# Optimization experiments

Hardware: AMD Instinct MI355X
Metric: run time of the kernel (lower is better)

## Reference

```python
import jax, jax.numpy as jnp
import numpy as np

N = 20000      # nodes
E = 320000     # edges (avg in-degree 16)
R = 100        # relation types
F = 256        # in_ent_feats == out_ent_feats == in_rel_feats
H = 8          # heads
D = F // H     # head dim = 32
HOP = 5        # PPR hops
ALPHA = 0.1
SLOPE = 0.2    # LeakyReLU negative slope


def _ln(x, g, b, eps=1e-5):
    m = x.mean(-1, keepdims=True)
    v = ((x - m) ** 2).mean(-1, keepdims=True)
    return (x - m) / jnp.sqrt(v + eps) * g + b


def setup_inputs() -> dict:
    key = jax.random.key(0)
    ks = jax.random.split(key, 12)
    s = 1.0 / np.sqrt(F)
    ent_feat = jax.random.normal(ks[0], (N, F), jnp.float32)
    rel_feat = jax.random.normal(ks[1], (R, F), jnp.float32)
    W_head = jax.random.normal(ks[2], (F, F), jnp.float32) * s
    W_tail = jax.random.normal(ks[3], (F, F), jnp.float32) * s
    W_ent = jax.random.normal(ks[4], (F, F), jnp.float32) * s
    W_rel = jax.random.normal(ks[5], (F, F), jnp.float32) * s
    attn = jax.random.normal(ks[6], (1, H, D), jnp.float32) * s
    ln_ent_g = jnp.ones((F,), jnp.float32); ln_ent_b = jnp.zeros((F,), jnp.float32)
    ln_rel_g = jnp.ones((F,), jnp.float32); ln_rel_b = jnp.zeros((F,), jnp.float32)
    ln_ff_g = jnp.ones((F,), jnp.float32); ln_ff_b = jnp.zeros((F,), jnp.float32)
    W1 = jax.random.normal(ks[7], (F, 4 * F), jnp.float32) * s
    b1 = jnp.zeros((4 * F,), jnp.float32)
    W2 = jax.random.normal(ks[8], (4 * F, F), jnp.float32) * (0.5 * s)
    b2 = jnp.zeros((F,), jnp.float32)
    src = jax.random.randint(ks[9], (E,), 0, N, dtype=jnp.int32)
    # every node must have in-degree >= 1 (DGL raises on 0-in-degree nodes)
    dst = jnp.concatenate([jnp.arange(N, dtype=jnp.int32),
                           jax.random.randint(ks[10], (E - N,), 0, N, dtype=jnp.int32)])
    rid = jax.random.randint(ks[11], (E,), 0, R, dtype=jnp.int32)
    return {"ent_feat": ent_feat, "rel_feat": rel_feat,
            "W_head": W_head, "W_tail": W_tail, "W_ent": W_ent, "W_rel": W_rel,
            "attn": attn,
            "ln_ent_g": ln_ent_g, "ln_ent_b": ln_ent_b,
            "ln_rel_g": ln_rel_g, "ln_rel_b": ln_rel_b,
            "ln_ff_g": ln_ff_g, "ln_ff_b": ln_ff_b,
            "W1": W1, "b1": b1, "W2": W2, "b2": b2,
            "src": src, "dst": dst, "rid": rid}


def reference(ent_feat, rel_feat, W_head, W_tail, W_ent, W_rel, attn,
              ln_ent_g, ln_ent_b, ln_rel_g, ln_rel_b, ln_ff_g, ln_ff_b,
              W1, b1, W2, b2, src, dst, rid):
    n = ent_feat.shape[0]
    x = _ln(ent_feat, ln_ent_g, ln_ent_b)                 # [N,F]
    fh = (x @ W_head).reshape(n, H, D)                    # 'eh'
    ftl = (x @ W_tail).reshape(n, H, D)                   # 'et'
    fen = (x @ W_ent).reshape(n, H, D)                    # 'ft'
    r = _ln(rel_feat, ln_rel_g, ln_rel_b)
    fr = (r @ W_rel).reshape(-1, H, D)[rid]               # [E,H,D]
    # relational edge attention score
    e = jax.nn.leaky_relu(fh[src] * ftl[dst] * fr, SLOPE)
    e = (e * attn).sum(-1)                                # [E,H]
    # e_mul_v with log in-degree, scaled by head_dim
    deg = jax.ops.segment_sum(jnp.ones((src.shape[0],), e.dtype), dst, num_segments=n)
    e = e * (jnp.log(deg)[dst])[:, None] / D
    # edge softmax over incoming edges of each dst node, per head
    m = jax.lax.stop_gradient(jax.ops.segment_max(e, dst, num_segments=n))
    ex = jnp.exp(e - m[dst])
    denom = jax.ops.segment_sum(ex, dst, num_segments=n)
    a = ex / denom[dst]                                   # [E,H]
    # PPR-style diffusion aggregation
    feat0 = fen
    feat = fen
    for _ in range(HOP):
        msg = feat[src] * a[:, :, None]                   # [E,H,D]
        agg = jax.ops.segment_sum(msg, dst, num_segments=n)
        feat = (1.0 - ALPHA) * agg + ALPHA * feat0
    # residual (Identity since in_ent_feats == out_ent_feats)
    rst = feat + ent_feat.reshape(n, H, D)
    rst = rst.reshape(n, F)
    # position-wise feed-forward with pre-LN and residual
    y = _ln(rst, ln_ff_g, ln_ff_b)
    ff = jax.nn.relu(y @ W1 + b1) @ W2 + b2
    return ff + rst
```

## Files before the change

kernel.cpp:

```cpp
#include <hip/hip_runtime.h>

#define N_NODES 20000
#define N_EDGES 320000
#define N_REL   100
#define FDIM    256
#define NHEAD   8
#define HDIM    32
#define SCAN_BLOCKS ((N_NODES + 255) / 256)

using short8 = __attribute__((ext_vector_type(8))) short;
using f32x4  = __attribute__((ext_vector_type(4))) float;

__device__ inline unsigned short f2bf(float f) {
    union { float f; unsigned int u; } v; v.f = f;
    unsigned int r = v.u + 0x7fff + ((v.u >> 16) & 1);
    return (unsigned short)(r >> 16);
}
__device__ inline float bf2f(unsigned short u) {
    union { unsigned int i; float f; } v; v.i = ((unsigned int)u) << 16; return v.f;
}
__device__ inline float4 bf4(ushort4 u) {
    return make_float4(bf2f(u.x), bf2f(u.y), bf2f(u.z), bf2f(u.w));
}
__device__ inline void unpack8(float* d, uint4 u) {
    union { unsigned int u; float f; } t;
    t.u = u.x << 16;         d[0] = t.f;
    t.u = u.x & 0xffff0000u; d[1] = t.f;
    t.u = u.y << 16;         d[2] = t.f;
    t.u = u.y & 0xffff0000u; d[3] = t.f;
    t.u = u.z << 16;         d[4] = t.f;
    t.u = u.z & 0xffff0000u; d[5] = t.f;
    t.u = u.w << 16;         d[6] = t.f;
    t.u = u.w & 0xffff0000u; d[7] = t.f;
}
__device__ inline void fma8(float* acc, uint4 u, float w) {
    union { unsigned int u; float f; } t;
    t.u = u.x << 16;         acc[0] += w * t.f;
    t.u = u.x & 0xffff0000u; acc[1] += w * t.f;
    t.u = u.y << 16;         acc[2] += w * t.f;
    t.u = u.y & 0xffff0000u; acc[3] += w * t.f;
    t.u = u.z << 16;         acc[4] += w * t.f;
    t.u = u.z & 0xffff0000u; acc[5] += w * t.f;
    t.u = u.w << 16;         acc[6] += w * t.f;
    t.u = u.w & 0xffff0000u; acc[7] += w * t.f;
}
__device__ __forceinline__ void g2lds16(const unsigned short* g, unsigned short* l) {
    __builtin_amdgcn_global_load_lds(
        (const __attribute__((address_space(1))) unsigned int*)g,
        (__attribute__((address_space(3))) unsigned int*)l,
        16, 0, 0);
}

__global__ __launch_bounds__(64) void ln_bf16_kernel(
    const float* __restrict__ in, const float* __restrict__ g,
    const float* __restrict__ b, unsigned short* __restrict__ out, int rows)
{
    int row = blockIdx.x;
    if (row >= rows) return;
    int tid = threadIdx.x;
    const float4 v = *(const float4*)(in + (size_t)row * FDIM + tid * 4);
    float s = v.x + v.y + v.z + v.w;
    float q = v.x * v.x + v.y * v.y + v.z * v.z + v.w * v.w;
    #pragma unroll
    for (int d = 1; d < 64; d <<= 1) { s += __shfl_xor(s, d); q += __shfl_xor(q, d); }
    float mean = s * (1.0f / FDIM);
    float var  = q * (1.0f / FDIM) - mean * mean;
    float inv  = rsqrtf(var + 1e-5f);
    float4 gg = *(const float4*)(g + tid * 4);
    float4 bb = *(const float4*)(b + tid * 4);
    ushort4 o;
    o.x = f2bf((v.x - mean) * inv * gg.x + bb.x);
    o.y = f2bf((v.y - mean) * inv * gg.y + bb.y);
    o.z = f2bf((v.z - mean) * inv * gg.z + bb.z);
    o.w = f2bf((v.w - mean) * inv * gg.w + bb.w);
    *(ushort4*)(out + (size_t)row * FDIM + tid * 4) = o;
}

__global__ __launch_bounds__(64) void rst_ln_kernel(
    const unsigned short* __restrict__ feat, const float* __restrict__ ent,
    const float* __restrict__ g, const float* __restrict__ b,
    float* __restrict__ rst, unsigned short* __restrict__ y)
{
    int row = blockIdx.x;
    int tid = threadIdx.x;
    const float4 f = bf4(*(const ushort4*)(feat + (size_t)row * FDIM + tid * 4));
    const float4 e = *(const float4*)(ent + (size_t)row * FDIM + tid * 4);
    float4 r;
    r.x = f.x + e.x; r.y = f.y + e.y; r.z = f.z + e.z; r.w = f.w + e.w;
    *(float4*)(rst + (size_t)row * FDIM + tid * 4) = r;
    float s = r.x + r.y + r.z + r.w;
    float q = r.x * r.x + r.y * r.y + r.z * r.z + r.w * r.w;
    #pragma unroll
    for (int d = 1; d < 64; d <<= 1) { s += __shfl_xor(s, d); q += __shfl_xor(q, d); }
    float mean = s * (1.0f / FDIM);
    float var  = q * (1.0f / FDIM) - mean * mean;
    float inv  = rsqrtf(var + 1e-5f);
    float4 gg = *(const float4*)(g + tid * 4);
    float4 bb = *(const float4*)(b + tid * 4);
    ushort4 o;
    o.x = f2bf((r.x - mean) * inv * gg.x + bb.x);
    o.y = f2bf((r.y - mean) * inv * gg.y + bb.y);
    o.z = f2bf((r.z - mean) * inv * gg.z + bb.z);
    o.w = f2bf((r.w - mean) * inv * gg.w + bb.w);
    *(ushort4*)(y + (size_t)row * FDIM + tid * 4) = o;
}

__global__ void transpose_bf16_kernel(const float* __restrict__ W,
                                      unsigned short* __restrict__ Wt, int K, int N)
{
    int idx = blockIdx.x * 256 + threadIdx.x;
    if (idx >= K * N) return;
    int n = idx / K, k = idx - n * K;
    Wt[idx] = f2bf(W[(size_t)k * N + n]);
}

__global__ __launch_bounds__(256) void mfma_gemm_bt(
    const unsigned short* __restrict__ A, const unsigned short* __restrict__ Bt,
    const float* __restrict__ bias, const float* __restrict__ add,
    float* __restrict__ Cf, unsigned short* __restrict__ Cb,
    int M, int K, int N, int relu)
{
    __shared__ unsigned short As[128 * 32];
    __shared__ unsigned short Bs[128 * 32];
    int tid  = threadIdx.x;
    int wave = tid >> 6, lane = tid & 63;
    int quad = lane >> 4, l16 = lane & 15;
    int m0 = blockIdx.x * 128, n0 = blockIdx.y * 128;
    int wr = (wave >> 1) * 64, wc = (wave & 1) * 64;

    f32x4 acc[4][4] = {};

    int cA = tid, cB = tid + 256;
    int rA0 = cA >> 2, kA0 = (cA & 3) * 8;
    int rB0 = cB >> 2, kB0 = (cB & 3) * 8;
    int rA = m0 + rA0; if (rA >= M) rA = M - 1;
    int rB = m0 + rB0; if (rB >= M) rB = M - 1;
    const unsigned short* gA0 = A + (size_t)rA * K + kA0;
    const unsigned short* gA1 = A + (size_t)rB * K + kB0;
    const unsigned short* gB0 = Bt + (size_t)(n0 + rA0) * K + kA0;
    const unsigned short* gB1 = Bt + (size_t)(n0 + rB0) * K + kB0;

    for (int k0 = 0; k0 < K; k0 += 32) {
        g2lds16(gA0 + k0, As + cA * 8);
        g2lds16(gA1 + k0, As + cB * 8);
        g2lds16(gB0 + k0, Bs + cA * 8);
        g2lds16(gB1 + k0, Bs + cB * 8);
        __syncthreads();
        short8 af[4], bfr[4];
        #pragma unroll
        for (int i = 0; i < 4; ++i)
            af[i] = *(const short8*)(As + (wr + i * 16 + l16) * 32 + quad * 8);
        #pragma unroll
        for (int j = 0; j < 4; ++j)
            bfr[j] = *(const short8*)(Bs + (wc + j * 16 + l16) * 32 + quad * 8);
        #pragma unroll
        for (int i = 0; i < 4; ++i)
            #pragma unroll
            for (int j = 0; j < 4; ++j)
                acc[i][j] = __builtin_amdgcn_mfma_f32_16x16x32_bf16(
                    af[i], bfr[j], acc[i][j], 0, 0, 0);
        __syncthreads();
    }

    #pragma unroll
    for (int i = 0; i < 4; ++i) {
        #pragma unroll
        for (int j = 0; j < 4; ++j) {
            int col = n0 + wc + j * 16 + l16;
            float bsv = bias ? bias[col] : 0.0f;
            #pragma unroll
            for (int r = 0; r < 4; ++r) {
                int row = m0 + wr + i * 16 + quad * 4 + r;
                if (row < M) {
                    float v = acc[i][j][r] + bsv;
                    if (relu) v = fmaxf(v, 0.0f);
                    if (add)  v += add[(size_t)row * N + col];
                    if (Cf) Cf[(size_t)row * N + col] = v;
                    else    Cb[(size_t)row * N + col] = f2bf(v);
                }
            }
        }
    }
}

__global__ __launch_bounds__(256) void mfma_gemm64_bt(
    const unsigned short* __restrict__ A, const unsigned short* __restrict__ Bt,
    const float* __restrict__ bias, const float* __restrict__ add,
    float* __restrict__ Cf, int M, int K, int N)
{
    __shared__ unsigned short As[64 * 32];
    __shared__ unsigned short Bs[128 * 32];
    int tid  = threadIdx.x;
    int wave = tid >> 6, lane = tid & 63;
    int quad = lane >> 4, l16 = lane & 15;
    int m0 = blockIdx.x * 64, n0 = blockIdx.y * 128;
    int wc = wave * 32;

    f32x4 acc[4][2] = {};

    int rA0 = tid >> 2, kA0 = (tid & 3) * 8;
    int cB0 = tid, cB1 = tid + 256;
    int rB0 = cB0 >> 2, kB0 = (cB0 & 3) * 8;
    int rB1 = cB1 >> 2, kB1 = (cB1 & 3) * 8;
    int rA = m0 + rA0; if (rA >= M) rA = M - 1;
    const unsigned short* gA  = A + (size_t)rA * K + kA0;
    const unsigned short* gB0 = Bt + (size_t)(n0 + rB0) * K + kB0;
    const unsigned short* gB1 = Bt + (size_t)(n0 + rB1) * K + kB1;

    for (int k0 = 0; k0 < K; k0 += 32) {
        g2lds16(gA + k0,  As + tid * 8);
        g2lds16(gB0 + k0, Bs + cB0 * 8);
        g2lds16(gB1 + k0, Bs + cB1 * 8);
        __syncthreads();
        short8 af[4], bfr[2];
        #pragma unroll
        for (int i = 0; i < 4; ++i)
            af[i] = *(const short8*)(As + (i * 16 + l16) * 32 + quad * 8);
        #pragma unroll
        for (int j = 0; j < 2; ++j)
            bfr[j] = *(const short8*)(Bs + (wc + j * 16 + l16) * 32 + quad * 8);
        #pragma unroll
        for (int i = 0; i < 4; ++i)
            #pragma unroll
            for (int j = 0; j < 2; ++j)
                acc[i][j] = __builtin_amdgcn_mfma_f32_16x16x32_bf16(
                    af[i], bfr[j], acc[i][j], 0, 0, 0);
        __syncthreads();
    }

    #pragma unroll
    for (int i = 0; i < 4; ++i) {
        #pragma unroll
        for (int j = 0; j < 2; ++j) {
            int col = n0 + wc + j * 16 + l16;
            float bsv = bias ? bias[col] : 0.0f;
            #pragma unroll
            for (int r = 0; r < 4; ++r) {
                int row = m0 + i * 16 + quad * 4 + r;
                if (row < M) {
                    float v = acc[i][j][r] + bsv;
                    if (add) v += add[(size_t)row * N + col];
                    Cf[(size_t)row * N + col] = v;
                }
            }
        }
    }
}

__global__ void count_kernel(const int* __restrict__ dst, int* __restrict__ deg, int E)
{
    int i = blockIdx.x * blockDim.x + threadIdx.x;
    if (i < E) atomicAdd(&deg[dst[i]], 1);
}

__global__ __launch_bounds__(256) void scan1_kernel(
    const int* __restrict__ deg, int* __restrict__ offsets, int* __restrict__ bsum, int n)
{
    __shared__ int tmp[256];
    int tid = threadIdx.x;
    int i = blockIdx.x * 256 + tid;
    int v = (i < n) ? deg[i] : 0;
    tmp[tid] = v;
    __syncthreads();
    for (int d = 1; d < 256; d <<= 1) {
        int u = (tid >= d) ? tmp[tid - d] : 0;
        __syncthreads();
        tmp[tid] += u;
        __syncthreads();
    }
    if (i < n) offsets[i] = tmp[tid] - v;
    if (tid == 255) bsum[blockIdx.x] = tmp[255];
}

__global__ __launch_bounds__(128) void scan2_kernel(int* __restrict__ bsum, int nb)
{
    __shared__ int tmp[128];
    int tid = threadIdx.x;
    int v = (tid < nb) ? bsum[tid] : 0;
    tmp[tid] = v;
    __syncthreads();
    for (int d = 1; d < 128; d <<= 1) {
        int u = (tid >= d) ? tmp[tid - d] : 0;
        __syncthreads();
        tmp[tid] += u;
        __syncthreads();
    }
    if (tid < nb) bsum[tid] = tmp[tid] - v;
}

__global__ __launch_bounds__(256) void scan3_kernel(
    const int* __restrict__ deg, int* __restrict__ offsets,
    const int* __restrict__ bsum, int* __restrict__ cursor,
    float* __restrict__ logdeg, int n, int E)
{
    int i = blockIdx.x * 256 + threadIdx.x;
    if (i < n) {
        int o = offsets[i] + bsum[blockIdx.x];
        offsets[i] = o;
        cursor[i]  = o;
        logdeg[i]  = logf((float)deg[i]);
    }
    if (i == 0) offsets[n] = E;
}

__global__ void scatter_kernel(const int* __restrict__ dst, const int* __restrict__ src,
                               const int* __restrict__ rid, int* __restrict__ cursor,
                               int* __restrict__ csr_src, int* __restrict__ csr_rid, int E)
{
    int i = blockIdx.x * blockDim.x + threadIdx.x;
    if (i < E) {
        int p = atomicAdd(&cursor[dst[i]], 1);
        csr_src[p] = src[i];
        csr_rid[p] = rid[i];
    }
}

__global__ __launch_bounds__(256) void edge_score_csr_kernel(
    const unsigned short* __restrict__ proj,
    const unsigned short* __restrict__ frel,
    const float* __restrict__ attn,
    const int* __restrict__ csr_src, const int* __restrict__ csr_rid,
    const int* __restrict__ offsets, const float* __restrict__ logdeg,
    float* __restrict__ csr_a, int n)
{
    int node = blockIdx.x * 4 + (threadIdx.x >> 6);
    if (node >= n) return;
    int tid = threadIdx.x & 63;
    int g = tid >> 4, li = tid & 15;
    int start = offsets[node], end = offsets[node + 1];
    float scale = logdeg[node] * (1.0f / 32.0f);

    float tv[16], at[16];
    {
        const unsigned short* tp = proj + (size_t)node * 768 + 256 + li * 16;
        uint4 a0 = *(const uint4*)tp, a1 = *(const uint4*)(tp + 8);
        unpack8(tv, a0); unpack8(tv + 8, a1);
        const float4* ap = (const float4*)(attn + li * 16);
        float4 f;
        f = ap[0]; at[0] = f.x; at[1] = f.y; at[2]  = f.z; at[3]  = f.w;
        f = ap[1]; at[4] = f.x; at[5] = f.y; at[6]  = f.z; at[7]  = f.w;
        f = ap[2]; at[8] = f.x; at[9] = f.y; at[10] = f.z; at[11] = f.w;
        f = ap[3]; at[12] = f.x; at[13] = f.y; at[14] = f.z; at[15] = f.w;
    }

    float denom = 0.f;
    for (int p = start; p < end; p += 8) {
        int  pe[2]; bool va[2]; uint4 h0[2], h1[2], r0[2], r1[2];
        #pragma unroll
        for (int t = 0; t < 2; ++t) {
            pe[t] = p + t * 4 + g;
            va[t] = pe[t] < end;
            int q = va[t] ? pe[t] : end - 1;
            int s = csr_src[q], r = csr_rid[q];
            const unsigned short* hp = proj + (size_t)s * 768 + li * 16;
            const unsigned short* rp = frel + (size_t)r * FDIM + li * 16;
            h0[t] = *(const uint4*)hp; h1[t] = *(const uint4*)(hp + 8);
            r0[t] = *(const uint4*)rp; r1[t] = *(const uint4*)(rp + 8);
        }
        #pragma unroll
        for (int t = 0; t < 2; ++t) {
            float hv[16], rv[16];
            unpack8(hv, h0[t]); unpack8(hv + 8, h1[t]);
            unpack8(rv, r0[t]); unpack8(rv + 8, r1[t]);
            float sum = 0.f;
            #pragma unroll
            for (int k = 0; k < 16; ++k) {
                float m = hv[k] * tv[k] * rv[k];
                m = (m > 0.f) ? m : 0.2f * m;
                sum += m * at[k];
            }
            sum += __shfl_xor(sum, 1);
            float ex = expf(sum * scale);
            if (va[t] && ((li & 1) == 0)) {
                csr_a[(size_t)pe[t] * NHEAD + (li >> 1)] = ex;
                denom += ex;
            }
        }
    }
    denom += __shfl_xor(denom, 16);
    denom += __shfl_xor(denom, 32);
    float dh = __shfl(denom, 2 * (tid & 7));
    for (int i = start * NHEAD + tid; i < end * NHEAD; i += 64)
        csr_a[i] = csr_a[i] / dh;
}

__global__ __launch_bounds__(256) void diffuse_kernel(
    const unsigned short* __restrict__ fin, int fin_stride,
    const unsigned short* __restrict__ feat0,
    const float* __restrict__ a, const int* __restrict__ csr_src,
    const int* __restrict__ offsets, unsigned short* __restrict__ fout, int n)
{
    int node = blockIdx.x * 4 + (threadIdx.x >> 6);
    if (node >= n) return;
    int tid = threadIdx.x & 63;
    int g = tid >> 4, li = tid & 15;
    int hh = li >> 1;
    int start = offsets[node], end = offsets[node + 1];
    float acc[16] = {};

    for (int p = start; p < end; p += 16) {
        uint4 u0[4], u1[4]; float w[4];
        #pragma unroll
        for (int t = 0; t < 4; ++t) {
            int pe = p + t * 4 + g;
            int q = (pe < end) ? pe : end - 1;
            int s = csr_src[q];
            w[t] = (pe < end) ? a[(size_t)q * NHEAD + hh] : 0.0f;
            const unsigned short* rp = fin + (size_t)s * fin_stride + li * 16;
            u0[t] = *(const uint4*)(rp);
            u1[t] = *(const uint4*)(rp + 8);
        }
        #pragma unroll
        for (int t = 0; t < 4; ++t) {
            fma8(acc + 0, u0[t], w[t]);
            fma8(acc + 8, u1[t], w[t]);
        }
    }
    #pragma unroll
    for (int k = 0; k < 16; ++k) {
        acc[k] += __shfl_xor(acc[k], 16);
        acc[k] += __shfl_xor(acc[k], 32);
    }
    if (g == 0) {
        const unsigned short* f0p = feat0 + (size_t)node * 768 + li * 16;
        uint4 f0a = *(const uint4*)(f0p);
        uint4 f0b = *(const uint4*)(f0p + 8);
        float f0[16];
        unpack8(f0, f0a); unpack8(f0 + 8, f0b);
        unsigned short o[16];
        #pragma unroll
        for (int k = 0; k < 16; ++k) o[k] = f2bf(0.9f * acc[k] + 0.1f * f0[k]);
        uint4* dst4 = (uint4*)(fout + (size_t)node * FDIM + li * 16);
        dst4[0] = *(uint4*)(o);
        dst4[1] = *(uint4*)(o + 8);
    }
}

extern "C" void kernel_launch(void* const* d_in, const int* in_sizes, int n_in,
                              void* d_out, int out_size, void* d_ws, size_t ws_size,
                              hipStream_t stream)
{
    const float* ent_feat = (const float*)d_in[0];
    const float* rel_feat = (const float*)d_in[1];
    const float* W_head   = (const float*)d_in[2];
    const float* W_tail   = (const float*)d_in[3];
    const float* W_ent    = (const float*)d_in[4];
    const float* W_rel    = (const float*)d_in[5];
    const float* attn     = (const float*)d_in[6];
    const float* ln_ent_g = (const float*)d_in[7];
    const float* ln_ent_b = (const float*)d_in[8];
    const float* ln_rel_g = (const float*)d_in[9];
    const float* ln_rel_b = (const float*)d_in[10];
    const float* ln_ff_g  = (const float*)d_in[11];
    const float* ln_ff_b  = (const float*)d_in[12];
    const float* W1       = (const float*)d_in[13];
    const float* b1       = (const float*)d_in[14];
    const float* W2       = (const float*)d_in[15];
    const float* b2       = (const float*)d_in[16];
    const int*   src      = (const int*)d_in[17];
    const int*   dst      = (const int*)d_in[18];
    const int*   rid      = (const int*)d_in[19];
    float* out = (float*)d_out;

    char* base = (char*)d_ws;
    auto carve = [&](size_t bytes) { char* p = base; base += (bytes + 255) & ~(size_t)255; return p; };
    unsigned short* xb    = (unsigned short*)carve((size_t)N_NODES * FDIM * 2);
    unsigned short* projb = (unsigned short*)carve((size_t)N_NODES * 768 * 2);
    unsigned short* rlnb  = (unsigned short*)carve((size_t)N_REL * FDIM * 2);
    unsigned short* frelb = (unsigned short*)carve((size_t)N_REL * FDIM * 2);
    unsigned short* WtP   = (unsigned short*)carve((size_t)768 * FDIM * 2);
    unsigned short* WtR   = (unsigned short*)carve((size_t)FDIM * FDIM * 2);
    unsigned short* W1t   = (unsigned short*)carve((size_t)1024 * FDIM * 2);
    unsigned short* W2t   = (unsigned short*)carve((size_t)FDIM * 1024 * 2);
    unsigned short* hb0   = (unsigned short*)carve((size_t)N_NODES * FDIM * 2);
    unsigned short* hb1   = (unsigned short*)carve((size_t)N_NODES * FDIM * 2);
    unsigned short* yb    = (unsigned short*)carve((size_t)N_NODES * FDIM * 2);
    unsigned short* t1b   = (unsigned short*)carve((size_t)N_NODES * 1024 * 2);
    float* rst     = (float*)carve((size_t)N_NODES * FDIM * 4);
    float* csr_a   = (float*)carve(((size_t)N_EDGES * NHEAD + 256) * 4);
    int*   csr_src = (int*)carve((size_t)(N_EDGES + 64) * 4);
    int*   csr_rid = (int*)carve((size_t)(N_EDGES + 64) * 4);
    int*   deg     = (int*)carve((size_t)N_NODES * 4);
    float* logdeg  = (float*)carve((size_t)N_NODES * 4);
    int*   offsets = (int*)carve((size_t)(N_NODES + 1) * 4);
    int*   cursor  = (int*)carve((size_t)N_NODES * 4);
    int*   bsum    = (int*)carve((size_t)SCAN_BLOCKS * 4);

    hipMemsetAsync(deg, 0, (size_t)N_NODES * 4, stream);

    ln_bf16_kernel<<<N_NODES, 64, 0, stream>>>(ent_feat, ln_ent_g, ln_ent_b, xb, N_NODES);
    ln_bf16_kernel<<<N_REL, 64, 0, stream>>>(rel_feat, ln_rel_g, ln_rel_b, rlnb, N_REL);

    transpose_bf16_kernel<<<(65536 + 255) / 256, 256, 0, stream>>>(W_head, WtP,              FDIM, FDIM);
    transpose_bf16_kernel<<<(65536 + 255) / 256, 256, 0, stream>>>(W_tail, WtP + 256 * FDIM, FDIM, FDIM);
    transpose_bf16_kernel<<<(65536 + 255) / 256, 256, 0, stream>>>(W_ent,  WtP + 512 * FDIM, FDIM, FDIM);
    transpose_bf16_kernel<<<(65536 + 255) / 256, 256, 0, stream>>>(W_rel,  WtR, FDIM, FDIM);
    transpose_bf16_kernel<<<(262144 + 255) / 256, 256, 0, stream>>>(W1, W1t, FDIM, 1024);
    transpose_bf16_kernel<<<(262144 + 255) / 256, 256, 0, stream>>>(W2, W2t, 1024, FDIM);

    dim3 gproj((N_NODES + 127) / 128, 768 / 128);
    mfma_gemm_bt<<<gproj, 256, 0, stream>>>(xb, WtP, nullptr, nullptr, nullptr, projb,
                                            N_NODES, FDIM, 768, 0);
    dim3 grel(1, FDIM / 128);
    mfma_gemm_bt<<<grel, 256, 0, stream>>>(rlnb, WtR, nullptr, nullptr, nullptr, frelb,
                                           N_REL, FDIM, FDIM, 0);

    count_kernel<<<(N_EDGES + 255) / 256, 256, 0, stream>>>(dst, deg, N_EDGES);
    scan1_kernel<<<SCAN_BLOCKS, 256, 0, stream>>>(deg, offsets, bsum, N_NODES);
    scan2_kernel<<<1, 128, 0, stream>>>(bsum, SCAN_BLOCKS);
    scan3_kernel<<<SCAN_BLOCKS, 256, 0, stream>>>(deg, offsets, bsum, cursor, logdeg,
                                                  N_NODES, N_EDGES);
    scatter_kernel<<<(N_EDGES + 255) / 256, 256, 0, stream>>>(dst, src, rid, cursor,
                                                              csr_src, csr_rid, N_EDGES);

    edge_score_csr_kernel<<<(N_NODES + 3) / 4, 256, 0, stream>>>(
        projb, frelb, attn, csr_src, csr_rid, offsets, logdeg, csr_a, N_NODES);

    const unsigned short* fen = projb + 512;
    int gdif = (N_NODES + 3) / 4;
    diffuse_kernel<<<gdif, 256, 0, stream>>>(fen, 768, fen, csr_a, csr_src, offsets, hb0, N_NODES);
    diffuse_kernel<<<gdif, 256, 0, stream>>>(hb0, FDIM, fen, csr_a, csr_src, offsets, hb1, N_NODES);
    diffuse_kernel<<<gdif, 256, 0, stream>>>(hb1, FDIM, fen, csr_a, csr_src, offsets, hb0, N_NODES);
    diffuse_kernel<<<gdif, 256, 0, stream>>>(hb0, FDIM, fen, csr_a, csr_src, offsets, hb1, N_NODES);
    diffuse_kernel<<<gdif, 256, 0, stream>>>(hb1, FDIM, fen, csr_a, csr_src, offsets, hb0, N_NODES);

    rst_ln_kernel<<<N_NODES, 64, 0, stream>>>(hb0, ent_feat, ln_ff_g, ln_ff_b, rst, yb);

    dim3 gff1((N_NODES + 127) / 128, 1024 / 128);
    mfma_gemm_bt<<<gff1, 256, 0, stream>>>(yb, W1t, b1, nullptr, nullptr, t1b,
                                           N_NODES, FDIM, 1024, 1);
    dim3 gff2((N_NODES + 63) / 64, FDIM / 128);
    mfma_gemm64_bt<<<gff2, 256, 0, stream>>>(t1b, W2t, b2, rst, out,
                                             N_NODES, 1024, FDIM);
}
```

Before: 506.4 us.

## Use head-major layouts for diffusion features and attention, split diffusion per head

Feature and attention buffers for the PPR diffusion are repacked into head-major layouts, and the diffusion kernel now runs one grid slice per head. Each per-head slice gathers only a 64-byte row segment, which may make the gather working set more cache friendly. The GEMMs also switch from direct global-to-LDS loads to register-staged loads, and FF1 uses the 64-row GEMM variant. These add a repack kernel and eight times more diffusion blocks, and give up the async LDS load path.

```diff
diff --git a/kernel.cpp b/kernel.cpp
--- a/kernel.cpp
+++ b/kernel.cpp
@@ -32,23 +32,6 @@
     t.u = u.z & 0xffff0000u; d[5] = t.f;
     t.u = u.w << 16;         d[6] = t.f;
     t.u = u.w & 0xffff0000u; d[7] = t.f;
-}
-__device__ inline void fma8(float* acc, uint4 u, float w) {
-    union { unsigned int u; float f; } t;
-    t.u = u.x << 16;         acc[0] += w * t.f;
-    t.u = u.x & 0xffff0000u; acc[1] += w * t.f;
-    t.u = u.y << 16;         acc[2] += w * t.f;
-    t.u = u.y & 0xffff0000u; acc[3] += w * t.f;
-    t.u = u.z << 16;         acc[4] += w * t.f;
-    t.u = u.z & 0xffff0000u; acc[5] += w * t.f;
-    t.u = u.w << 16;         acc[6] += w * t.f;
-    t.u = u.w & 0xffff0000u; acc[7] += w * t.f;
-}
-__device__ __forceinline__ void g2lds16(const unsigned short* g, unsigned short* l) {
-    __builtin_amdgcn_global_load_lds(
-        (const __attribute__((address_space(1))) unsigned int*)g,
-        (__attribute__((address_space(3))) unsigned int*)l,
-        16, 0, 0);
 }
 
 __global__ __launch_bounds__(64) void ln_bf16_kernel(
@@ -77,13 +60,15 @@
 }
 
 __global__ __launch_bounds__(64) void rst_ln_kernel(
-    const unsigned short* __restrict__ feat, const float* __restrict__ ent,
+    const unsigned short* __restrict__ featH, const float* __restrict__ ent,
     const float* __restrict__ g, const float* __restrict__ b,
     float* __restrict__ rst, unsigned short* __restrict__ y)
 {
     int row = blockIdx.x;
     int tid = threadIdx.x;
-    const float4 f = bf4(*(const ushort4*)(feat + (size_t)row * FDIM + tid * 4));
+    int h = tid >> 3;
+    const ushort4 fu = *(const ushort4*)(featH + ((size_t)h * N_NODES + row) * 32 + (tid & 7) * 4);
+    const float4 f = bf4(fu);
     const float4 e = *(const float4*)(ent + (size_t)row * FDIM + tid * 4);
     float4 r;
     r.x = f.x + e.x; r.y = f.y + e.y; r.z = f.z + e.z; r.w = f.w + e.w;
@@ -114,6 +99,18 @@
     Wt[idx] = f2bf(W[(size_t)k * N + n]);
 }
 
+__global__ void repack_fen_kernel(const unsigned short* __restrict__ projb,
+                                  unsigned short* __restrict__ F0, int n)
+{
+    int idx = blockIdx.x * 256 + threadIdx.x;
+    int total = n * 128;
+    if (idx >= total) return;
+    int row = idx >> 7, d2 = idx & 127;
+    int h = d2 >> 4, w = d2 & 15;
+    ((unsigned int*)F0)[((size_t)h * n + row) * 16 + w] =
+        ((const unsigned int*)projb)[(size_t)row * 384 + 256 + d2];
+}
+
 __global__ __launch_bounds__(256) void mfma_gemm_bt(
     const unsigned short* __restrict__ A, const unsigned short* __restrict__ Bt,
     const float* __restrict__ bias, const float* __restrict__ add,
@@ -141,10 +138,10 @@
     const unsigned short* gB1 = Bt + (size_t)(n0 + rB0) * K + kB0;
 
     for (int k0 = 0; k0 < K; k0 += 32) {
-        g2lds16(gA0 + k0, As + cA * 8);
-        g2lds16(gA1 + k0, As + cB * 8);
-        g2lds16(gB0 + k0, Bs + cA * 8);
-        g2lds16(gB1 + k0, Bs + cB * 8);
+        ((uint4*)As)[cA] = *(const uint4*)(gA0 + k0);
+        ((uint4*)As)[cB] = *(const uint4*)(gA1 + k0);
+        ((uint4*)Bs)[cA] = *(const uint4*)(gB0 + k0);
+        ((uint4*)Bs)[cB] = *(const uint4*)(gB1 + k0);
         __syncthreads();
         short8 af[4], bfr[4];
         #pragma unroll
@@ -186,7 +183,8 @@
 __global__ __launch_bounds__(256) void mfma_gemm64_bt(
     const unsigned short* __restrict__ A, const unsigned short* __restrict__ Bt,
     const float* __restrict__ bias, const float* __restrict__ add,
-    float* __restrict__ Cf, int M, int K, int N)
+    float* __restrict__ Cf, unsigned short* __restrict__ Cb,
+    int M, int K, int N, int relu)
 {
     __shared__ unsigned short As[64 * 32];
     __shared__ unsigned short Bs[128 * 32];
@@ -208,9 +206,9 @@
     const unsigned short* gB1 = Bt + (size_t)(n0 + rB1) * K + kB1;
 
     for (int k0 = 0; k0 < K; k0 += 32) {
-        g2lds16(gA + k0,  As + tid * 8);
-        g2lds16(gB0 + k0, Bs + cB0 * 8);
-        g2lds16(gB1 + k0, Bs + cB1 * 8);
+        ((uint4*)As)[tid] = *(const uint4*)(gA + k0);
+        ((uint4*)Bs)[cB0] = *(const uint4*)(gB0 + k0);
+        ((uint4*)Bs)[cB1] = *(const uint4*)(gB1 + k0);
         __syncthreads();
         short8 af[4], bfr[2];
         #pragma unroll
@@ -239,8 +237,10 @@
                 int row = m0 + i * 16 + quad * 4 + r;
                 if (row < M) {
                     float v = acc[i][j][r] + bsv;
-                    if (add) v += add[(size_t)row * N + col];
-                    Cf[(size_t)row * N + col] = v;
+                    if (relu) v = fmaxf(v, 0.0f);
+                    if (add)  v += add[(size_t)row * N + col];
+                    if (Cf) Cf[(size_t)row * N + col] = v;
+                    else    Cb[(size_t)row * N + col] = f2bf(v);
                 }
             }
         }
@@ -321,7 +321,7 @@
     const float* __restrict__ attn,
     const int* __restrict__ csr_src, const int* __restrict__ csr_rid,
     const int* __restrict__ offsets, const float* __restrict__ logdeg,
-    float* __restrict__ csr_a, int n)
+    float* __restrict__ aH, int n)
 {
     int node = blockIdx.x * 4 + (threadIdx.x >> 6);
     if (node >= n) return;
@@ -372,67 +372,63 @@
             sum += __shfl_xor(sum, 1);
             float ex = expf(sum * scale);
             if (va[t] && ((li & 1) == 0)) {
-                csr_a[(size_t)pe[t] * NHEAD + (li >> 1)] = ex;
+                aH[(size_t)(li >> 1) * N_EDGES + pe[t]] = ex;
                 denom += ex;
             }
         }
     }
     denom += __shfl_xor(denom, 16);
     denom += __shfl_xor(denom, 32);
-    float dh = __shfl(denom, 2 * (tid & 7));
-    for (int i = start * NHEAD + tid; i < end * NHEAD; i += 64)
-        csr_a[i] = csr_a[i] / dh;
-}
-
-__global__ __launch_bounds__(256) void diffuse_kernel(
-    const unsigned short* __restrict__ fin, int fin_stride,
+    #pragma unroll
+    for (int h2 = 0; h2 < 8; ++h2) {
+        float inv = 1.0f / __shfl(denom, 2 * h2);
+        for (int e = start + tid; e < end; e += 64)
+            aH[(size_t)h2 * N_EDGES + e] *= inv;
+    }
+}
+
+__global__ __launch_bounds__(256) void diffuse_h_kernel(
+    const unsigned short* __restrict__ fin,
     const unsigned short* __restrict__ feat0,
-    const float* __restrict__ a, const int* __restrict__ csr_src,
-    const int* __restrict__ offsets, unsigned short* __restrict__ fout, int n)
-{
-    int node = blockIdx.x * 4 + (threadIdx.x >> 6);
+    const float* __restrict__ aH,
+    const int* __restrict__ csr_src, const int* __restrict__ offsets,
+    unsigned short* __restrict__ fout, int n)
+{
+    int h = blockIdx.x & 7;
+    int node = (blockIdx.x >> 3) * 4 + (threadIdx.x >> 6);
     if (node >= n) return;
     int tid = threadIdx.x & 63;
     int g = tid >> 4, li = tid & 15;
-    int hh = li >> 1;
     int start = offsets[node], end = offsets[node + 1];
-    float acc[16] = {};
-
+    const unsigned int* finh = (const unsigned int*)fin + (size_t)h * n * 16;
+    const float* ah = aH + (size_t)h * N_EDGES;
+    float ax = 0.f, ay = 0.f;
     for (int p = start; p < end; p += 16) {
-        uint4 u0[4], u1[4]; float w[4];
+        unsigned int u[4]; float w[4];
         #pragma unroll
         for (int t = 0; t < 4; ++t) {
             int pe = p + t * 4 + g;
             int q = (pe < end) ? pe : end - 1;
             int s = csr_src[q];
-            w[t] = (pe < end) ? a[(size_t)q * NHEAD + hh] : 0.0f;
-            const unsigned short* rp = fin + (size_t)s * fin_stride + li * 16;
-            u0[t] = *(const uint4*)(rp);
-            u1[t] = *(const uint4*)(rp + 8);
+            w[t] = (pe < end) ? ah[q] : 0.0f;
+            u[t] = finh[s * 16 + li];
         }
         #pragma unroll
         for (int t = 0; t < 4; ++t) {
-            fma8(acc + 0, u0[t], w[t]);
-            fma8(acc + 8, u1[t], w[t]);
+            union { unsigned int u; float f; } lo, hi;
+            lo.u = u[t] << 16; hi.u = u[t] & 0xffff0000u;
+            ax += w[t] * lo.f; ay += w[t] * hi.f;
         }
     }
-    #pragma unroll
-    for (int k = 0; k < 16; ++k) {
-        acc[k] += __shfl_xor(acc[k], 16);
-        acc[k] += __shfl_xor(acc[k], 32);
-    }
+    ax += __shfl_xor(ax, 16); ax += __shfl_xor(ax, 32);
+    ay += __shfl_xor(ay, 16); ay += __shfl_xor(ay, 32);
     if (g == 0) {
-        const unsigned short* f0p = feat0 + (size_t)node * 768 + li * 16;
-        uint4 f0a = *(const uint4*)(f0p);
-        uint4 f0b = *(const uint4*)(f0p + 8);
-        float f0[16];
-        unpack8(f0, f0a); unpack8(f0 + 8, f0b);
-        unsigned short o[16];
-        #pragma unroll
-        for (int k = 0; k < 16; ++k) o[k] = f2bf(0.9f * acc[k] + 0.1f * f0[k]);
-        uint4* dst4 = (uint4*)(fout + (size_t)node * FDIM + li * 16);
-        dst4[0] = *(uint4*)(o);
-        dst4[1] = *(uint4*)(o + 8);
+        unsigned int f0 = ((const unsigned int*)feat0)[((size_t)h * n + node) * 16 + li];
+        union { unsigned int u; float f; } lo, hi;
+        lo.u = f0 << 16; hi.u = f0 & 0xffff0000u;
+        unsigned int o = (unsigned int)f2bf(0.9f * ax + 0.1f * lo.f)
+                       | ((unsigned int)f2bf(0.9f * ay + 0.1f * hi.f) << 16);
+        ((unsigned int*)fout)[((size_t)h * n + node) * 16 + li] = o;
     }
 }
 
@@ -472,12 +468,13 @@
     unsigned short* WtR   = (unsigned short*)carve((size_t)FDIM * FDIM * 2);
     unsigned short* W1t   = (unsigned short*)carve((size_t)1024 * FDIM * 2);
     unsigned short* W2t   = (unsigned short*)carve((size_t)FDIM * 1024 * 2);
-    unsigned short* hb0   = (unsigned short*)carve((size_t)N_NODES * FDIM * 2);
-    unsigned short* hb1   = (unsigned short*)carve((size_t)N_NODES * FDIM * 2);
+    unsigned short* F0H   = (unsigned short*)carve((size_t)N_NODES * FDIM * 2);
+    unsigned short* hbH0  = (unsigned short*)carve((size_t)N_NODES * FDIM * 2);
+    unsigned short* hbH1  = (unsigned short*)carve((size_t)N_NODES * FDIM * 2);
     unsigned short* yb    = (unsigned short*)carve((size_t)N_NODES * FDIM * 2);
     unsigned short* t1b   = (unsigned short*)carve((size_t)N_NODES * 1024 * 2);
     float* rst     = (float*)carve((size_t)N_NODES * FDIM * 4);
-    float* csr_a   = (float*)carve(((size_t)N_EDGES * NHEAD + 256) * 4);
+    float* aH      = (float*)carve((size_t)N_EDGES * NHEAD * 4);
     int*   csr_src = (int*)carve((size_t)(N_EDGES + 64) * 4);
     int*   csr_rid = (int*)carve((size_t)(N_EDGES + 64) * 4);
     int*   deg     = (int*)carve((size_t)N_NODES * 4);
@@ -505,6 +502,8 @@
     mfma_gemm_bt<<<grel, 256, 0, stream>>>(rlnb, WtR, nullptr, nullptr, nullptr, frelb,
                                            N_REL, FDIM, FDIM, 0);
 
+    repack_fen_kernel<<<(N_NODES * 128 + 255) / 256, 256, 0, stream>>>(projb, F0H, N_NODES);
+
     count_kernel<<<(N_EDGES + 255) / 256, 256, 0, stream>>>(dst, deg, N_EDGES);
     scan1_kernel<<<SCAN_BLOCKS, 256, 0, stream>>>(deg, offsets, bsum, N_NODES);
     scan2_kernel<<<1, 128, 0, stream>>>(bsum, SCAN_BLOCKS);
@@ -514,22 +513,21 @@
                                                               csr_src, csr_rid, N_EDGES);
 
     edge_score_csr_kernel<<<(N_NODES + 3) / 4, 256, 0, stream>>>(
-        projb, frelb, attn, csr_src, csr_rid, offsets, logdeg, csr_a, N_NODES);
-
-    const unsigned short* fen = projb + 512;
-    int gdif = (N_NODES + 3) / 4;
-    diffuse_kernel<<<gdif, 256, 0, stream>>>(fen, 768, fen, csr_a, csr_src, offsets, hb0, N_NODES);
-    diffuse_kernel<<<gdif, 256, 0, stream>>>(hb0, FDIM, fen, csr_a, csr_src, offsets, hb1, N_NODES);
-    diffuse_kernel<<<gdif, 256, 0, stream>>>(hb1, FDIM, fen, csr_a, csr_src, offsets, hb0, N_NODES);
-    diffuse_kernel<<<gdif, 256, 0, stream>>>(hb0, FDIM, fen, csr_a, csr_src, offsets, hb1, N_NODES);
-    diffuse_kernel<<<gdif, 256, 0, stream>>>(hb1, FDIM, fen, csr_a, csr_src, offsets, hb0, N_NODES);
-
-    rst_ln_kernel<<<N_NODES, 64, 0, stream>>>(hb0, ent_feat, ln_ff_g, ln_ff_b, rst, yb);
-
-    dim3 gff1((N_NODES + 127) / 128, 1024 / 128);
-    mfma_gemm_bt<<<gff1, 256, 0, stream>>>(yb, W1t, b1, nullptr, nullptr, t1b,
-                                           N_NODES, FDIM, 1024, 1);
+        projb, frelb, attn, csr_src, csr_rid, offsets, logdeg, aH, N_NODES);
+
+    int gdif = ((N_NODES + 3) / 4) * 8;
+    diffuse_h_kernel<<<gdif, 256, 0, stream>>>(F0H,  F0H, aH, csr_src, offsets, hbH0, N_NODES);
+    diffuse_h_kernel<<<gdif, 256, 0, stream>>>(hbH0, F0H, aH, csr_src, offsets, hbH1, N_NODES);
+    diffuse_h_kernel<<<gdif, 256, 0, stream>>>(hbH1, F0H, aH, csr_src, offsets, hbH0, N_NODES);
+    diffuse_h_kernel<<<gdif, 256, 0, stream>>>(hbH0, F0H, aH, csr_src, offsets, hbH1, N_NODES);
+    diffuse_h_kernel<<<gdif, 256, 0, stream>>>(hbH1, F0H, aH, csr_src, offsets, hbH0, N_NODES);
+
+    rst_ln_kernel<<<N_NODES, 64, 0, stream>>>(hbH0, ent_feat, ln_ff_g, ln_ff_b, rst, yb);
+
+    dim3 gff1((N_NODES + 63) / 64, 1024 / 128);
+    mfma_gemm64_bt<<<gff1, 256, 0, stream>>>(yb, W1t, b1, nullptr, nullptr, t1b,
+                                             N_NODES, FDIM, 1024, 1);
     dim3 gff2((N_NODES + 63) / 64, FDIM / 128);
-    mfma_gemm64_bt<<<gff2, 256, 0, stream>>>(t1b, W2t, b2, rst, out,
-                                             N_NODES, 1024, FDIM);
-}
+    mfma_gemm64_bt<<<gff2, 256, 0, stream>>>(t1b, W2t, b2, rst, out, nullptr,
+                                             N_NODES, 1024, FDIM, 0);
+}
```

Result: slower. 697.8 us (+37.8%).
